# Kernel optimization log

Measured on AMD Instinct MI355X. Metric: run time of the kernel, lower is better.

## Reference

```python
import jax, jax.numpy as jnp
import numpy as np

B, H, W, DIM, HEADS = 4, 32, 32, 768, 12
HD = DIM // HEADS


def setup_inputs() -> dict:
    key = jax.random.key(0)
    ks = jax.random.split(key, 5)
    return {
        "x": jax.random.normal(ks[0], (B, H, W, DIM), jnp.float32),
        "qkv_w": jax.random.normal(ks[1], (3 * DIM, DIM), jnp.float32) * 0.02,
        "qkv_b": jnp.zeros((3 * DIM,), jnp.float32),
        "proj_w": jax.random.normal(ks[2], (DIM, DIM), jnp.float32) * 0.02,
        "proj_b": jnp.zeros((DIM,), jnp.float32),
        "rel_pos_h": jax.random.normal(ks[3], (2 * H - 1, HD), jnp.float32) * 0.02,
        "rel_pos_w": jax.random.normal(ks[4], (2 * W - 1, HD), jnp.float32) * 0.02,
    }


def reference(x, qkv_w, qkv_b, proj_w, proj_b, rel_pos_h, rel_pos_w):
    b, h, w, dim = x.shape
    heads = HEADS
    hd = dim // heads
    n = h * w
    scale = hd ** -0.5

    xf = x.reshape(b, n, dim)
    qkv = xf @ qkv_w.T + qkv_b                          # [b, n, 3*dim]
    qkv = qkv.reshape(b, n, 3, heads, hd)
    qkv = jnp.transpose(qkv, (2, 0, 3, 1, 4)).reshape(3, b * heads, n, hd)
    q, k, v = qkv[0], qkv[1], qkv[2]                    # [b*heads, n, hd]

    # decomposed relative position bias (q_size == k_size, no interpolation)
    idx_h = jnp.arange(h)[:, None] - jnp.arange(h)[None, :] + (h - 1)
    idx_w = jnp.arange(w)[:, None] - jnp.arange(w)[None, :] + (w - 1)
    Rh = rel_pos_h[idx_h]                               # [h, h, hd]
    Rw = rel_pos_w[idx_w]                               # [w, w, hd]
    r_q = q.reshape(b * heads, h, w, hd)
    rel_h = jnp.einsum('bhwc,hkc->bhwk', r_q, Rh)       # [bH, h, w, h]
    rel_w = jnp.einsum('bhwc,wkc->bhwk', r_q, Rw)       # [bH, h, w, w]
    bias = (rel_h[:, :, :, :, None] + rel_w[:, :, :, None, :]).reshape(b * heads, n, n)

    attn = jax.nn.softmax(jnp.einsum('bnd,bmd->bnm', q * scale, k) + bias, axis=-1)
    out = jnp.einsum('bnm,bmd->bnd', attn, v)           # [b*heads, n, hd]
    out = out.reshape(b, heads, n, hd).transpose(0, 2, 1, 3).reshape(b, n, dim)
    out = out @ proj_w.T + proj_b
    return out.reshape(b, h, w, dim)
```

## Files before the change

### kernel.cpp

```cpp
#include <hip/hip_runtime.h>

#define DEV_INLINE static __device__ __forceinline__

typedef __attribute__((ext_vector_type(8))) short bf16x8;
typedef __attribute__((ext_vector_type(4))) float f32x4;
typedef __attribute__((ext_vector_type(16))) float f32x16;

DEV_INLINE unsigned short f2bf(float f) {
  union { float f; unsigned int u; } v; v.f = f;
  unsigned int u = v.u;
  u += 0x7FFFu + ((u >> 16) & 1u);
  return (unsigned short)(u >> 16);
}
DEV_INLINE float bf2f(unsigned short h) {
  union { unsigned int u; float f; } v; v.u = ((unsigned int)h) << 16; return v.f;
}

__global__ __launch_bounds__(256) void cvt_f32_bf16(const float* __restrict__ in,
                                                    unsigned short* __restrict__ out, int n4) {
  int i = blockIdx.x * 256 + threadIdx.x;
  if (i >= n4) return;
  float4 v = reinterpret_cast<const float4*>(in)[i];
  ushort4 o;
  o.x = f2bf(v.x); o.y = f2bf(v.y); o.z = f2bf(v.z); o.w = f2bf(v.w);
  reinterpret_cast<ushort4*>(out)[i] = o;
}

template <int MODE>
__global__ __launch_bounds__(256) void gemm_bf16(const unsigned short* __restrict__ A,
                                                 const unsigned short* __restrict__ Bw,
                                                 const float* __restrict__ bias,
                                                 float* __restrict__ outF,
                                                 unsigned short* __restrict__ qo,
                                                 unsigned short* __restrict__ ko,
                                                 unsigned short* __restrict__ vo) {
  __shared__ unsigned short As[128 * 40];
  __shared__ unsigned short Bs[128 * 40];

  const int tid = threadIdx.x;
  const int lane = tid & 63;
  const int wv = tid >> 6;
  const int wrow = (wv >> 1) * 64;
  const int wcol = (wv & 1) * 64;
  const int m0 = blockIdx.y * 128;
  const int n0 = blockIdx.x * 128;
  const int l15 = lane & 15;
  const int lg = lane >> 4;
  const int koff = lg * 8;

  f32x4 acc[4][4];
#pragma unroll
  for (int i = 0; i < 4; ++i)
#pragma unroll
    for (int j = 0; j < 4; ++j) acc[i][j] = (f32x4){0.f, 0.f, 0.f, 0.f};

  for (int kt = 0; kt < 768; kt += 32) {
    __syncthreads();
#pragma unroll
    for (int i = 0; i < 2; ++i) {
      int s = tid + i * 256;
      int row = s >> 2, sc = (s & 3) * 8;
      *reinterpret_cast<int4*>(&As[row * 40 + sc]) =
          *reinterpret_cast<const int4*>(&A[(m0 + row) * 768 + kt + sc]);
      *reinterpret_cast<int4*>(&Bs[row * 40 + sc]) =
          *reinterpret_cast<const int4*>(&Bw[(n0 + row) * 768 + kt + sc]);
    }
    __syncthreads();

    bf16x8 aF[4], bF[4];
#pragma unroll
    for (int i = 0; i < 4; ++i)
      aF[i] = *reinterpret_cast<const bf16x8*>(&As[(wrow + i * 16 + l15) * 40 + koff]);
#pragma unroll
    for (int j = 0; j < 4; ++j)
      bF[j] = *reinterpret_cast<const bf16x8*>(&Bs[(wcol + j * 16 + l15) * 40 + koff]);
#pragma unroll
    for (int i = 0; i < 4; ++i)
#pragma unroll
      for (int j = 0; j < 4; ++j)
        acc[i][j] = __builtin_amdgcn_mfma_f32_16x16x32_bf16(aF[i], bF[j], acc[i][j], 0, 0, 0);
  }

#pragma unroll
  for (int i = 0; i < 4; ++i) {
#pragma unroll
    for (int j = 0; j < 4; ++j) {
#pragma unroll
      for (int r = 0; r < 4; ++r) {
        int row = m0 + wrow + i * 16 + lg * 4 + r;
        int col = n0 + wcol + j * 16 + l15;
        float val = acc[i][j][r] + bias[col];
        if (MODE == 0) {
          int t = col / 768;
          int rem = col - t * 768;
          int head = rem >> 6;
          int c = rem & 63;
          int bb = row >> 10;
          int n = row & 1023;
          if (t == 1) val *= 0.125f;
          unsigned short* dst = (t == 0) ? qo : (t == 1) ? ko : vo;
          dst[((bb * 12 + head) * 1024 + n) * 64 + c] = f2bf(val);
        } else {
          outF[row * 768 + col] = val;
        }
      }
    }
  }
}

__global__ __launch_bounds__(256) void vtrans(const unsigned short* __restrict__ vb,
                                              unsigned short* __restrict__ vt) {
  __shared__ unsigned short t[64][72];
  const int n0 = blockIdx.x * 64;
  const int bh = blockIdx.y;
  const int tid = threadIdx.x;
#pragma unroll
  for (int i = 0; i < 4; ++i) {
    int s = tid + i * 256;
    int row = s >> 4, c4 = (s & 15) * 4;
    *reinterpret_cast<ushort4*>(&t[row][c4]) =
        *reinterpret_cast<const ushort4*>(&vb[(bh * 1024 + n0 + row) * 64 + c4]);
  }
  __syncthreads();
#pragma unroll
  for (int i = 0; i < 4; ++i) {
    int s = tid + i * 256;
    int d = s >> 4, n4 = (s & 15) * 4;
    ushort4 o;
    o.x = t[n4 + 0][d]; o.y = t[n4 + 1][d]; o.z = t[n4 + 2][d]; o.w = t[n4 + 3][d];
    *reinterpret_cast<ushort4*>(&vt[(bh * 64 + d) * 1024 + n0 + n4]) = o;
  }
}

DEV_INLINE f32x4 mfma16(bf16x8 a, bf16x8 b, f32x4 c) {
  return __builtin_amdgcn_mfma_f32_16x16x32_bf16(a, b, c, 0, 0, 0);
}

__global__ __launch_bounds__(64) void rel_mfma16(const unsigned short* __restrict__ q,
                                                 const float* __restrict__ rph,
                                                 const float* __restrict__ rpw,
                                                 unsigned short* __restrict__ relwb,
                                                 float* __restrict__ relh) {
  __shared__ unsigned short qs[32 * 72];
  __shared__ unsigned short rhh[32 * 72], rhl[32 * 72];
  __shared__ unsigned short rwh[64 * 72], rwl[64 * 72];
  __shared__ float relh_s[32 * 36];
  __shared__ unsigned short relw_s[32 * 40];

  const int lane = threadIdx.x;
  const int l15 = lane & 15;
  const int lg = lane >> 4;
  const int qh = blockIdx.x;
  const int bh = blockIdx.y;

#pragma unroll
  for (int it = 0; it < 4; ++it) {
    int s = lane + it * 64;
    int row = s >> 3, ch = s & 7;
    *reinterpret_cast<int4*>(&qs[row * 72 + ch * 8]) =
        *reinterpret_cast<const int4*>(&q[(bh * 1024 + qh * 32 + row) * 64 + ch * 8]);
  }
#pragma unroll
  for (int it = 0; it < 8; ++it) {
    int s = lane + it * 64;
    int row = s >> 4, c4 = (s & 15) * 4;
    float4 v = *reinterpret_cast<const float4*>(&rph[(qh + row) * 64 + c4]);
    ushort4 h, l;
    h.x = f2bf(v.x); l.x = f2bf(v.x - bf2f(h.x));
    h.y = f2bf(v.y); l.y = f2bf(v.y - bf2f(h.y));
    h.z = f2bf(v.z); l.z = f2bf(v.z - bf2f(h.z));
    h.w = f2bf(v.w); l.w = f2bf(v.w - bf2f(h.w));
    *reinterpret_cast<ushort4*>(&rhh[row * 72 + c4]) = h;
    *reinterpret_cast<ushort4*>(&rhl[row * 72 + c4]) = l;
  }
#pragma unroll
  for (int it = 0; it < 16; ++it) {
    int s = lane + it * 64;
    int row = s >> 4, c4 = (s & 15) * 4;
    float4 v = (float4){0.f, 0.f, 0.f, 0.f};
    if (row < 63) v = *reinterpret_cast<const float4*>(&rpw[row * 64 + c4]);
    ushort4 h, l;
    h.x = f2bf(v.x); l.x = f2bf(v.x - bf2f(h.x));
    h.y = f2bf(v.y); l.y = f2bf(v.y - bf2f(h.y));
    h.z = f2bf(v.z); l.z = f2bf(v.z - bf2f(h.z));
    h.w = f2bf(v.w); l.w = f2bf(v.w - bf2f(h.w));
    *reinterpret_cast<ushort4*>(&rwh[row * 72 + c4]) = h;
    *reinterpret_cast<ushort4*>(&rwl[row * 72 + c4]) = l;
  }
  __syncthreads();

  const int k0 = lg * 8, k1 = 32 + lg * 8;
  bf16x8 fq[2][2], fhh[2][2], fhl[2][2], fwh[4][2], fwl[4][2];
#pragma unroll
  for (int t = 0; t < 2; ++t) {
    fq[t][0]  = *reinterpret_cast<const bf16x8*>(&qs[(t * 16 + l15) * 72 + k0]);
    fq[t][1]  = *reinterpret_cast<const bf16x8*>(&qs[(t * 16 + l15) * 72 + k1]);
    fhh[t][0] = *reinterpret_cast<const bf16x8*>(&rhh[(t * 16 + l15) * 72 + k0]);
    fhh[t][1] = *reinterpret_cast<const bf16x8*>(&rhh[(t * 16 + l15) * 72 + k1]);
    fhl[t][0] = *reinterpret_cast<const bf16x8*>(&rhl[(t * 16 + l15) * 72 + k0]);
    fhl[t][1] = *reinterpret_cast<const bf16x8*>(&rhl[(t * 16 + l15) * 72 + k1]);
  }
#pragma unroll
  for (int t = 0; t < 4; ++t) {
    fwh[t][0] = *reinterpret_cast<const bf16x8*>(&rwh[(t * 16 + l15) * 72 + k0]);
    fwh[t][1] = *reinterpret_cast<const bf16x8*>(&rwh[(t * 16 + l15) * 72 + k1]);
    fwl[t][0] = *reinterpret_cast<const bf16x8*>(&rwl[(t * 16 + l15) * 72 + k0]);
    fwl[t][1] = *reinterpret_cast<const bf16x8*>(&rwl[(t * 16 + l15) * 72 + k1]);
  }

  f32x4 ah[2][2];
#pragma unroll
  for (int i = 0; i < 2; ++i)
#pragma unroll
    for (int jj = 0; jj < 2; ++jj) {
      f32x4 a = (f32x4){0.f, 0.f, 0.f, 0.f};
      a = mfma16(fhh[i][0], fq[jj][0], a);
      a = mfma16(fhh[i][1], fq[jj][1], a);
      a = mfma16(fhl[i][0], fq[jj][0], a);
      a = mfma16(fhl[i][1], fq[jj][1], a);
      ah[i][jj] = a;
    }
  f32x4 aw[2][4];
#pragma unroll
  for (int i = 0; i < 2; ++i)
#pragma unroll
    for (int jj = 0; jj < 4; ++jj) {
      f32x4 a = (f32x4){0.f, 0.f, 0.f, 0.f};
      a = mfma16(fq[i][0], fwh[jj][0], a);
      a = mfma16(fq[i][1], fwh[jj][1], a);
      a = mfma16(fq[i][0], fwl[jj][0], a);
      a = mfma16(fq[i][1], fwl[jj][1], a);
      aw[i][jj] = a;
    }

#pragma unroll
  for (int i = 0; i < 2; ++i)
#pragma unroll
    for (int jj = 0; jj < 2; ++jj)
#pragma unroll
      for (int r = 0; r < 4; ++r) {
        int t = i * 16 + lg * 4 + r;
        int qw = jj * 16 + l15;
        relh_s[qw * 36 + 31 - t] = ah[i][jj][r];
      }
#pragma unroll
  for (int i = 0; i < 2; ++i)
#pragma unroll
    for (int jj = 0; jj < 4; ++jj)
#pragma unroll
      for (int r = 0; r < 4; ++r) {
        int qw = i * 16 + lg * 4 + r;
        int d = jj * 16 + l15;
        int kw = qw + 31 - d;
        if (kw >= 0 && kw < 32) relw_s[qw * 40 + kw] = f2bf(aw[i][jj][r]);
      }
  __syncthreads();

#pragma unroll
  for (int it = 0; it < 4; ++it) {
    int s = lane + it * 64;
    int row = s >> 3, c4 = (s & 7) * 4;
    *reinterpret_cast<float4*>(&relh[(bh * 1024 + qh * 32 + row) * 32 + c4]) =
        *reinterpret_cast<const float4*>(&relh_s[row * 36 + c4]);
  }
#pragma unroll
  for (int it = 0; it < 2; ++it) {
    int s = lane + it * 64;
    int row = s >> 2, ch = s & 3;
    *reinterpret_cast<int4*>(&relwb[(bh * 1024 + qh * 32 + row) * 32 + ch * 8]) =
        *reinterpret_cast<const int4*>(&relw_s[row * 40 + ch * 8]);
  }
}

DEV_INLINE f32x16 mfma32(bf16x8 a, bf16x8 b, f32x16 c) {
  return __builtin_amdgcn_mfma_f32_32x32x16_bf16(a, b, c, 0, 0, 0);
}

DEV_INLINE bf16x8 make_pa(const float* p) {
  unsigned int W0, W1, W2, W3;
  asm("v_cvt_pk_bf16_f32 %0, %1, %2" : "=v"(W0) : "v"(p[0]), "v"(p[1]));
  asm("v_cvt_pk_bf16_f32 %0, %1, %2" : "=v"(W1) : "v"(p[2]), "v"(p[3]));
  asm("v_cvt_pk_bf16_f32 %0, %1, %2" : "=v"(W2) : "v"(p[4]), "v"(p[5]));
  asm("v_cvt_pk_bf16_f32 %0, %1, %2" : "=v"(W3) : "v"(p[6]), "v"(p[7]));
  asm("v_permlane32_swap_b32 %0, %1" : "+v"(W0), "+v"(W2));
  asm("v_permlane32_swap_b32 %0, %1" : "+v"(W1), "+v"(W3));
  union { unsigned int w[4]; bf16x8 v; } u;
  u.w[0] = W0; u.w[1] = W1; u.w[2] = W2; u.w[3] = W3;
  return u.v;
}

__global__ __launch_bounds__(128) void attn2(const unsigned short* __restrict__ kg,
                                             const unsigned short* __restrict__ vtg,
                                             const unsigned short* __restrict__ qg,
                                             const unsigned short* __restrict__ relwb,
                                             const float* __restrict__ relh,
                                             unsigned short* __restrict__ ao) {
  __shared__ unsigned short k_lin[2][64 * 64];
  __shared__ unsigned short v_lin[2][64 * 64];

  const int tid = threadIdx.x;
  const int lane = tid & 63;
  const int wv = tid >> 6;
  const int l31 = lane & 31;
  const int hi = lane >> 5;

  const int bid = blockIdx.x;
  const int swz = (bid & 7) * 96 + (bid >> 3);
  const int bh = swz >> 4;
  const int qt = swz & 15;
  const int q0 = qt * 64 + wv * 32;

  bf16x8 qf[6];
  {
    const unsigned short* qrow = &qg[(bh * 1024 + q0 + l31) * 64 + hi * 8];
#pragma unroll
    for (int c = 0; c < 4; ++c)
      qf[c] = *reinterpret_cast<const bf16x8*>(&qrow[c * 16]);
    const unsigned short* wrow = &relwb[(bh * 1024 + q0 + l31) * 32 + hi * 8];
    qf[4] = *reinterpret_cast<const bf16x8*>(&wrow[0]);
    qf[5] = *reinterpret_cast<const bf16x8*>(&wrow[16]);
  }

  bf16x8 ohf0, ohf1;
  {
    int t0 = l31 - 8 * hi;
    int t1 = l31 - 16 - 8 * hi;
    union { unsigned int w[4]; bf16x8 v; } u0, u1;
#pragma unroll
    for (int w = 0; w < 4; ++w) {
      u0.w[w] = (t0 >= 0 && (t0 >> 1) == w) ? ((t0 & 1) ? 0x3F800000u : 0x3F80u) : 0u;
      u1.w[w] = (t1 >= 0 && (t1 >> 1) == w) ? ((t1 & 1) ? 0x3F800000u : 0x3F80u) : 0u;
    }
    ohf0 = u0.v; ohf1 = u1.v;
  }

  f32x16 O0, O1;
#pragma unroll
  for (int r = 0; r < 16; ++r) { O0[r] = 0.f; O1[r] = 0.f; }
  float m_r = -3.0e38f, l_r = 0.f;

  const int srow = lane >> 3;
  const int scb = (lane & 7) ^ srow;
  const int rsw = l31 & 7;

#define STAGE(KT, B)                                                                       \
  do {                                                                                     \
    _Pragma("unroll") for (int pp = 0; pp < 4; ++pp) {                                     \
      int p = wv * 4 + pp;                                                                 \
      int row = p * 8 + srow;                                                              \
      const unsigned short* gk = &kg[(bh * 1024 + (KT) * 64 + row) * 64 + scb * 8];        \
      __builtin_amdgcn_global_load_lds(                                                    \
          (const __attribute__((address_space(1))) unsigned int*)gk,                       \
          (__attribute__((address_space(3))) unsigned int*)&k_lin[B][p * 512], 16, 0, 0);  \
      const unsigned short* gv = &vtg[(bh * 64 + row) * 1024 + (KT) * 64 + scb * 8];       \
      __builtin_amdgcn_global_load_lds(                                                    \
          (const __attribute__((address_space(1))) unsigned int*)gv,                       \
          (__attribute__((address_space(3))) unsigned int*)&v_lin[B][p * 512], 16, 0, 0);  \
    }                                                                                      \
  } while (0)

  STAGE(0, 0);

  for (int kt = 0; kt < 16; ++kt) {
    const int b = kt & 1;
    __syncthreads();
    if (kt < 15) STAGE(kt + 1, b ^ 1);

    float2 bhv = *reinterpret_cast<const float2*>(&relh[(bh * 1024 + q0 + l31) * 32 + 2 * kt]);
    float bh0 = bhv.x, bh1 = bhv.y;

    f32x16 s0, s1;
#pragma unroll
    for (int r = 0; r < 16; ++r) { s0[r] = 0.f; s1[r] = 0.f; }
    {
      const unsigned short* kb0 = &k_lin[b][l31 * 64];
      const unsigned short* kb1 = &k_lin[b][(32 + l31) * 64];
#pragma unroll
      for (int c = 0; c < 4; ++c) {
        int cb = ((2 * c + hi) ^ rsw) * 8;
        s0 = mfma32(*reinterpret_cast<const bf16x8*>(&kb0[cb]), qf[c], s0);
        s1 = mfma32(*reinterpret_cast<const bf16x8*>(&kb1[cb]), qf[c], s1);
      }
      s0 = mfma32(ohf0, qf[4], s0);
      s0 = mfma32(ohf1, qf[5], s0);
      s1 = mfma32(ohf0, qf[4], s1);
      s1 = mfma32(ohf1, qf[5], s1);
    }

    float pm0 = s0[0], pm1 = s1[0];
#pragma unroll
    for (int r = 1; r < 16; ++r) { pm0 = fmaxf(pm0, s0[r]); pm1 = fmaxf(pm1, s1[r]); }
    float pmax = fmaxf(pm0 + bh0, pm1 + bh1);
    pmax = fmaxf(pmax, __shfl_xor(pmax, 32));

    if (!__all(pmax <= m_r + 8.f)) {
      float mnew = fmaxf(m_r, pmax);
      float corr = __expf(m_r - mnew);
      m_r = mnew;
      l_r *= corr;
#pragma unroll
      for (int r = 0; r < 16; ++r) {
        int cr = ((r & 3) + 8 * (r >> 2) + 4 * hi) << 2;
        float c2 = __int_as_float(__builtin_amdgcn_ds_bpermute(cr, __float_as_int(corr)));
        O0[r] *= c2;
        O1[r] *= c2;
      }
    }

    float mb0 = m_r - bh0, mb1 = m_r - bh1;
    float p0[16], p1[16];
    float ps = 0.f;
#pragma unroll
    for (int r = 0; r < 16; ++r) { p0[r] = __expf(s0[r] - mb0); ps += p0[r]; }
#pragma unroll
    for (int r = 0; r < 16; ++r) { p1[r] = __expf(s1[r] - mb1); ps += p1[r]; }
    ps += __shfl_xor(ps, 32);
    l_r += ps;

    bf16x8 pa0 = make_pa(p0 + 0);
    bf16x8 pa1 = make_pa(p0 + 8);
    bf16x8 pa2 = make_pa(p1 + 0);
    bf16x8 pa3 = make_pa(p1 + 8);

    const unsigned short* vb0 = &v_lin[b][l31 * 64];
    const unsigned short* vb1 = &v_lin[b][(32 + l31) * 64];
#pragma unroll
    for (int c = 0; c < 4; ++c) {
      bf16x8 pac = (c == 0) ? pa0 : (c == 1) ? pa1 : (c == 2) ? pa2 : pa3;
      int cb = ((2 * c + hi) ^ rsw) * 8;
      O0 = mfma32(pac, *reinterpret_cast<const bf16x8*>(&vb0[cb]), O0);
      O1 = mfma32(pac, *reinterpret_cast<const bf16x8*>(&vb1[cb]), O1);
    }
  }
#undef STAGE

  float invl = 1.f / l_r;
  const int bb = bh / 12, head = bh % 12;
#pragma unroll
  for (int r = 0; r < 16; ++r) {
    int crow = (r & 3) + 8 * (r >> 2) + 4 * hi;
    float il = __int_as_float(__builtin_amdgcn_ds_bpermute(crow << 2, __float_as_int(invl)));
    int n = q0 + crow;
    unsigned short* dst = &ao[(bb * 1024 + n) * 768 + head * 64];
    dst[l31] = f2bf(O0[r] * il);
    dst[32 + l31] = f2bf(O1[r] * il);
  }
}

extern "C" void kernel_launch(void* const* d_in, const int* in_sizes, int n_in,
                              void* d_out, int out_size, void* d_ws, size_t ws_size,
                              hipStream_t stream) {
  const float* x      = (const float*)d_in[0];
  const float* qkv_w  = (const float*)d_in[1];
  const float* qkv_b  = (const float*)d_in[2];
  const float* proj_w = (const float*)d_in[3];
  const float* proj_b = (const float*)d_in[4];
  const float* rph    = (const float*)d_in[5];
  const float* rpw    = (const float*)d_in[6];
  float* out = (float*)d_out;

  char* ws = (char*)d_ws;
  unsigned short* xb    = (unsigned short*)(ws);
  float*          relh  = (float*)(ws);
  unsigned short* wqkv  = (unsigned short*)(ws + 6291456);
  unsigned short* wproj = (unsigned short*)(ws + 9830400);
  unsigned short* qb    = (unsigned short*)(ws + 11010048);
  unsigned short* kb    = (unsigned short*)(ws + 17301504);
  unsigned short* vb    = (unsigned short*)(ws + 23592960);
  unsigned short* ao    = (unsigned short*)(ws + 23592960);
  unsigned short* vt    = (unsigned short*)(ws + 29884416);
  unsigned short* relwb = (unsigned short*)(ws + 36175872);

  cvt_f32_bf16<<<3072, 256, 0, stream>>>(x, xb, 786432);
  cvt_f32_bf16<<<1728, 256, 0, stream>>>(qkv_w, wqkv, 442368);
  cvt_f32_bf16<<<576, 256, 0, stream>>>(proj_w, wproj, 147456);

  gemm_bf16<0><<<dim3(18, 32), 256, 0, stream>>>(xb, wqkv, qkv_b, nullptr, qb, kb, vb);
  vtrans<<<dim3(16, 48), 256, 0, stream>>>(vb, vt);
  rel_mfma16<<<dim3(32, 48), 64, 0, stream>>>(qb, rph, rpw, relwb, relh);
  attn2<<<768, 128, 0, stream>>>(kb, vt, qb, relwb, relh, ao);
  gemm_bf16<1><<<dim3(6, 32), 256, 0, stream>>>(ao, wproj, proj_b, out, nullptr, nullptr, nullptr);
}
```

Measured before the change: 134.9 us.

## Double-buffer GEMM tiles with direct global-to-LDS loads and XOR swizzle

Replaces the register-staged, padded shared-memory tile loads in the bf16 GEMM with `global_load_lds` direct-to-LDS transfers into two LDS buffers. The next K-tile is prefetched while MFMAs run on the current one, leaving one barrier per iteration instead of two. An XOR swizzle on the 16-byte segments replaces the padding to avoid LDS bank conflicts. Correctness relies on the compiler waiting for the async LDS writes at the barrier.

```diff
diff --git a/kernel.cpp b/kernel.cpp
--- a/kernel.cpp
+++ b/kernel.cpp
@@ -34,8 +34,8 @@
                                                  unsigned short* __restrict__ qo,
                                                  unsigned short* __restrict__ ko,
                                                  unsigned short* __restrict__ vo) {
-  __shared__ unsigned short As[128 * 40];
-  __shared__ unsigned short Bs[128 * 40];
+  __shared__ unsigned short As[2][128 * 32];
+  __shared__ unsigned short Bs[2][128 * 32];
 
   const int tid = threadIdx.x;
   const int lane = tid & 63;
@@ -46,7 +46,9 @@
   const int n0 = blockIdx.x * 128;
   const int l15 = lane & 15;
   const int lg = lane >> 4;
-  const int koff = lg * 8;
+
+  const int srow = lane >> 2;
+  const int seg  = (lane & 3) ^ (srow & 3);
 
   f32x4 acc[4][4];
 #pragma unroll
@@ -54,32 +56,44 @@
 #pragma unroll
     for (int j = 0; j < 4; ++j) acc[i][j] = (f32x4){0.f, 0.f, 0.f, 0.f};
 
-  for (int kt = 0; kt < 768; kt += 32) {
+#define GSTAGE(KT, B)                                                                        \
+  do {                                                                                       \
+    _Pragma("unroll") for (int pp = 0; pp < 2; ++pp) {                                       \
+      int p = wv * 2 + pp;                                   \
+      int row = p * 16 + srow;                                                               \
+      const unsigned short* ga = &A[(m0 + row) * 768 + (KT) * 32 + seg * 8];                 \
+      __builtin_amdgcn_global_load_lds(                                                      \
+          (const __attribute__((address_space(1))) unsigned int*)ga,                         \
+          (__attribute__((address_space(3))) unsigned int*)&As[B][p * 512], 16, 0, 0);       \
+      const unsigned short* gb = &Bw[(n0 + row) * 768 + (KT) * 32 + seg * 8];                \
+      __builtin_amdgcn_global_load_lds(                                                      \
+          (const __attribute__((address_space(1))) unsigned int*)gb,                         \
+          (__attribute__((address_space(3))) unsigned int*)&Bs[B][p * 512], 16, 0, 0);       \
+    }                                                                                        \
+  } while (0)
+
+  GSTAGE(0, 0);
+
+  for (int kt = 0; kt < 24; ++kt) {
+    const int b = kt & 1;
     __syncthreads();
-#pragma unroll
-    for (int i = 0; i < 2; ++i) {
-      int s = tid + i * 256;
-      int row = s >> 2, sc = (s & 3) * 8;
-      *reinterpret_cast<int4*>(&As[row * 40 + sc]) =
-          *reinterpret_cast<const int4*>(&A[(m0 + row) * 768 + kt + sc]);
-      *reinterpret_cast<int4*>(&Bs[row * 40 + sc]) =
-          *reinterpret_cast<const int4*>(&Bw[(n0 + row) * 768 + kt + sc]);
-    }
-    __syncthreads();
-
+    if (kt < 23) GSTAGE(kt + 1, b ^ 1);
+
+    const int soff = (lg ^ (l15 & 3)) * 8;
     bf16x8 aF[4], bF[4];
 #pragma unroll
     for (int i = 0; i < 4; ++i)
-      aF[i] = *reinterpret_cast<const bf16x8*>(&As[(wrow + i * 16 + l15) * 40 + koff]);
+      aF[i] = *reinterpret_cast<const bf16x8*>(&As[b][(wrow + i * 16 + l15) * 32 + soff]);
 #pragma unroll
     for (int j = 0; j < 4; ++j)
-      bF[j] = *reinterpret_cast<const bf16x8*>(&Bs[(wcol + j * 16 + l15) * 40 + koff]);
+      bF[j] = *reinterpret_cast<const bf16x8*>(&Bs[b][(wcol + j * 16 + l15) * 32 + soff]);
 #pragma unroll
     for (int i = 0; i < 4; ++i)
 #pragma unroll
       for (int j = 0; j < 4; ++j)
         acc[i][j] = __builtin_amdgcn_mfma_f32_16x16x32_bf16(aF[i], bF[j], acc[i][j], 0, 0, 0);
   }
+#undef GSTAGE
 
 #pragma unroll
   for (int i = 0; i < 4; ++i) {
@@ -87,7 +101,7 @@
     for (int j = 0; j < 4; ++j) {
 #pragma unroll
       for (int r = 0; r < 4; ++r) {
-        int row = m0 + wrow + i * 16 + lg * 4 + r;
+        int row = m0 + wrow + i * 16 + (lane >> 4) * 4 + r;
         int col = n0 + wcol + j * 16 + l15;
         float val = acc[i][j][r] + bias[col];
         if (MODE == 0) {
```

Result: faster. 127.1 us (-5.8%).
